# Performance work log

Hardware: AMD Instinct MI355X
Metric: run time of the kernel (lower is better)

## Reference

```python
import jax, jax.numpy as jnp
import numpy as np

B, K_SLOTS, P = 4096, 8, 768
SLOT = P // 3          # 256, slot feature dim
HID = 256              # pres/up hidden width
NC, NP = 512, 512
LN_EPS = 1e-5


def _layernorm(x, g, b):
    m = jnp.mean(x, axis=-1, keepdims=True)
    v = jnp.var(x, axis=-1, keepdims=True)
    return (x - m) * jax.lax.rsqrt(v + LN_EPS) * g + b


def _mlp2(x, W1, b1, g, bt, W2, b2):
    # Linear -> LayerNorm -> ReLU -> Linear (torchvision ops.MLP with hidden=[256, out])
    h = jax.nn.relu(_layernorm(x @ W1 + b1, g, bt))
    return h @ W2 + b2


def setup_inputs() -> dict:
    key = jax.random.key(0)
    ks = jax.random.split(key, 24)
    rn = lambda k, shp, s=1.0: jax.random.normal(k, shp, dtype=jnp.float32) * s
    d = {
        "inst_embed": rn(ks[0], (B, P)),
        "slots": rn(ks[1], (B, K_SLOTS, SLOT)),
        # fc / fp: single Linear(p, p)
        "Wfc": rn(ks[2], (P, P), 1.0 / np.sqrt(P)),
        "bfc": jnp.zeros((P,), jnp.float32),
        "Wfp": rn(ks[3], (P, P), 1.0 / np.sqrt(P)),
        "bfp": jnp.zeros((P,), jnp.float32),
        # memory codebooks (plain randn per the original)
        "Kc": rn(ks[4], (NC, P)),
        "Vc": rn(ks[5], (NC, P)),
        "Kp": rn(ks[6], (NP, P)),
        "Vp": rn(ks[7], (NP, P)),
        # pres MLP: Linear(4p/3,256)+LN+ReLU, Linear(256,p/3)
        "pres_W1": rn(ks[8], (SLOT + P, HID), 1.0 / np.sqrt(SLOT + P)),
        "pres_b1": jnp.zeros((HID,), jnp.float32),
        "pres_g": jnp.ones((HID,), jnp.float32),
        "pres_bt": jnp.zeros((HID,), jnp.float32),
        "pres_W2": rn(ks[9], (HID, SLOT), 1.0 / np.sqrt(HID)),
        "pres_b2": jnp.zeros((SLOT,), jnp.float32),
        # up MLP: same shapes
        "up_W1": rn(ks[10], (SLOT + P, HID), 1.0 / np.sqrt(SLOT + P)),
        "up_b1": jnp.zeros((HID,), jnp.float32),
        "up_g": jnp.ones((HID,), jnp.float32),
        "up_bt": jnp.zeros((HID,), jnp.float32),
        "up_W2": rn(ks[11], (HID, SLOT), 1.0 / np.sqrt(HID)),
        "up_b2": jnp.zeros((SLOT,), jnp.float32),
    }
    return d


def reference(inst_embed, slots, Wfc, bfc, Wfp, bfp, Kc, Vc, Kp, Vp,
              pres_W1, pres_b1, pres_g, pres_bt, pres_W2, pres_b2,
              up_W1, up_b1, up_g, up_bt, up_W2, up_b2):
    scale = jnp.float32(np.sqrt(P))
    # selection: soft attention over the two codebooks
    Qc = inst_embed @ Wfc + bfc                     # [B, P]
    Qp = inst_embed @ Wfp + bfp                     # [B, P]
    c = jax.nn.softmax(jnp.einsum('bi,ci->bc', Qc, Kc) / scale, axis=-1) @ Vc  # [B, P]
    p = jax.nn.softmax(jnp.einsum('bi,pi->bp', Qp, Kp) / scale, axis=-1) @ Vp  # [B, P]
    # update: vectorized over the K slot loop of the original
    cb = jnp.broadcast_to(c[:, None, :], (B, K_SLOTS, P))
    pb = jnp.broadcast_to(p[:, None, :], (B, K_SLOTS, P))
    hc = jnp.concatenate([slots, cb], axis=-1)      # [B, K, SLOT+P]
    hp = jnp.concatenate([slots, pb], axis=-1)      # [B, K, SLOT+P]
    gate_pres = _mlp2(hc, pres_W1, pres_b1, pres_g, pres_bt, pres_W2, pres_b2)
    gate_up = _mlp2(hp, up_W1, up_b1, up_g, up_bt, up_W2, up_b2)
    return slots + gate_pres * gate_up              # [B, K, SLOT]
```

## Files before the change

kernel.cpp:

```cpp
#include <hip/hip_runtime.h>
#include <stdint.h>

#define BB    4096
#define KS    8
#define PP    768
#define SLOT  256
#define HID   256
#define NC    512
#define BKROWS (BB*KS)
typedef unsigned short u16;
typedef short bf16x8 __attribute__((ext_vector_type(8)));
typedef float f32x4  __attribute__((ext_vector_type(4)));

__device__ __forceinline__ u16 f2bf(float x) {
  union { float f; uint32_t u; } v; v.f = x;
  return (u16)((v.u + 0x7FFFu + ((v.u >> 16) & 1u)) >> 16);
}

__device__ __forceinline__ u16 f2h(float x) {
  union { _Float16 h; u16 u; } cv; cv.h = (_Float16)x; return cv.u;
}
__device__ __forceinline__ float h2f(u16 x) {
  union { u16 u; _Float16 h; } cv; cv.u = x; return (float)cv.h;
}

__device__ __forceinline__ void gload_lds16(u16* ldst, const u16* gsrc) {
  __builtin_amdgcn_global_load_lds(
      (const __attribute__((address_space(1))) void*)gsrc,
      (__attribute__((address_space(3))) void*)ldst, 16, 0, 0);
}

template<int EPI>
__device__ __forceinline__ void gemm_core64(
    const u16* __restrict__ A, int lda,
    const u16* __restrict__ B, int ldb,
    const float* __restrict__ bias,
    void* __restrict__ out, int ldo, int K,
    int blockRow, int blockCol, u16* lsA, u16* lsB)
{
  const int tid  = threadIdx.x;
  const int w    = tid >> 6;
  const int lane = tid & 63;
  const int wm   = w >> 1, wn = w & 1;
  const int rl   = lane >> 4, cl = lane & 15;

  f32x4 acc[2][4];
  const f32x4 zero = {0.f, 0.f, 0.f, 0.f};
#pragma unroll
  for (int i = 0; i < 2; ++i)
#pragma unroll
    for (int j = 0; j < 4; ++j) acc[i][j] = zero;

  const u16* Ablk = A + (size_t)blockRow * lda;
  const u16* Bblk = B + (size_t)blockCol * ldb;

  for (int k0 = 0; k0 < K; k0 += 64) {
#pragma unroll
    for (int i = 0; i < 2; ++i) {
      int seg   = i * 4 + w;
      int off16 = seg * 64 + lane;
      int row   = off16 >> 3;
      int chunk = (off16 & 7) ^ (row & 7);
      gload_lds16(lsA + seg * 512, Ablk + (size_t)row * lda + k0 + chunk * 8);
    }
#pragma unroll
    for (int i = 0; i < 4; ++i) {
      int seg   = i * 4 + w;
      int off16 = seg * 64 + lane;
      int row   = off16 >> 3;
      int chunk = (off16 & 7) ^ (row & 7);
      gload_lds16(lsB + seg * 512, Bblk + (size_t)row * ldb + k0 + chunk * 8);
    }
    __syncthreads();

#pragma unroll
    for (int ks = 0; ks < 2; ++ks) {
      bf16x8 aF[2], bF[4];
#pragma unroll
      for (int f = 0; f < 2; ++f) {
        int r  = wm * 32 + f * 16 + cl;
        int ca = ((ks * 4 + rl) ^ (r & 7)) * 8;
        aF[f] = *(const bf16x8*)(lsA + r * 64 + ca);
      }
#pragma unroll
      for (int f = 0; f < 4; ++f) {
        int rn = wn * 64 + f * 16 + cl;
        int cb = ((ks * 4 + rl) ^ (rn & 7)) * 8;
        bF[f] = *(const bf16x8*)(lsB + rn * 64 + cb);
      }
#pragma unroll
      for (int fm = 0; fm < 2; ++fm)
#pragma unroll
        for (int fn = 0; fn < 4; ++fn)
          acc[fm][fn] = __builtin_amdgcn_mfma_f32_16x16x32_bf16(
              aF[fm], bF[fn], acc[fm][fn], 0, 0, 0);
    }
    __syncthreads();
  }

#pragma unroll
  for (int fm = 0; fm < 2; ++fm) {
#pragma unroll
    for (int fn = 0; fn < 4; ++fn) {
      f32x4 v = acc[fm][fn];
#pragma unroll
      for (int r = 0; r < 4; ++r) {
        int grow = blockRow + wm * 32 + fm * 16 + rl * 4 + r;
        int gcol = blockCol + wn * 64 + fn * 16 + cl;
        float x = v[r];
        if constexpr (EPI == 2) {
          ((u16*)out)[(size_t)grow * ldo + gcol] = f2bf(x);
        } else if constexpr (EPI == 3) {
          x += bias[gcol];
          ((float*)out)[(size_t)grow * ldo + gcol] = x;
        } else if constexpr (EPI == 5) {
          x += bias[gcol];
          ((u16*)out)[(size_t)grow * ldo + gcol] = f2h(x);
        }
      }
    }
  }
}

__device__ __forceinline__ void cvt_seg(const float* __restrict__ in,
                                        u16* __restrict__ outp, int b, int n4) {
  int i = b * 256 + threadIdx.x;
  if (i < n4) {
    float4 v = ((const float4*)in)[i];
    ushort4 o;
    o.x = f2bf(v.x); o.y = f2bf(v.y); o.z = f2bf(v.z); o.w = f2bf(v.w);
    ((ushort4*)outp)[i] = o;
  }
}

__device__ __forceinline__ void pack_seg(const float* __restrict__ s0,
                                         const float* __restrict__ s1,
                                         u16* __restrict__ dst, int b) {
  int br = b >> 4, ng = b & 15;
  const float* src = br ? s1 : s0;
  int w = threadIdx.x >> 6, lane = threadIdx.x & 63;
  int rl = lane >> 4, cl = lane & 15;
#pragma unroll
  for (int s = 0; s < 2; ++s) {
    int step = w * 2 + s;
    union { u16 u[8]; uint4 q; } o;
#pragma unroll
    for (int j = 0; j < 8; ++j)
      o.u[j] = f2bf(src[(size_t)(step * 32 + rl * 8 + j) * 256 + ng * 16 + cl]);
    *(uint4*)(dst + (size_t)(((br * 16 + ng) * 8 + step) * 64 + lane) * 8) = o.q;
  }
}

__global__ __launch_bounds__(256) void prep_all(
    const float* __restrict__ inst, const float* __restrict__ Kc,
    const float* __restrict__ Kp, const float* __restrict__ Wfc,
    const float* __restrict__ Wfp, const float* __restrict__ Vc,
    const float* __restrict__ Vp, const float* __restrict__ pW1,
    const float* __restrict__ uW1, const float* __restrict__ pW2,
    const float* __restrict__ uW2, const float* __restrict__ bfc,
    const float* __restrict__ bfp,
    u16* instb, u16* Kcb, u16* Kpb, u16* Wfcb, u16* Wfpb, u16* Vcb, u16* Vpb,
    u16* W1Tp, u16* W1Tu, u16* W1pk, u16* W2pk, float* sb)
{
  __shared__ float tile[32][33];
  int b = blockIdx.x;
  if (b < 3072)      { cvt_seg(inst, instb, b,        786432); return; }
  else if (b < 3456) { cvt_seg(Kc,   Kcb,   b - 3072,  98304); return; }
  else if (b < 3840) { cvt_seg(Kp,   Kpb,   b - 3456,  98304); return; }
  else if (b < 4416) { cvt_seg(Wfc,  Wfcb,  b - 3840, 147456); return; }
  else if (b < 4992) { cvt_seg(Wfp,  Wfpb,  b - 4416, 147456); return; }
  else if (b < 5376) { cvt_seg(Vc,   Vcb,   b - 4992,  98304); return; }
  else if (b < 5760) { cvt_seg(Vp,   Vpb,   b - 5376,  98304); return; }
  else if (b < 6272) {
    int bb = b - 5760;
    const float* in = (bb < 256) ? pW1 : uW1;
    u16* outp = (bb < 256) ? W1Tp : W1Tu;
    bb &= 255;
    int tc = (bb & 7) * 32, tr = (bb >> 3) * 32;
    int lx = threadIdx.x & 31, ly = threadIdx.x >> 5;
#pragma unroll
    for (int i = 0; i < 32; i += 8)
      tile[ly + i][lx] = in[(size_t)(tr + ly + i) * 256 + tc + lx];
    __syncthreads();
#pragma unroll
    for (int i = 0; i < 32; i += 8)
      outp[(size_t)(tc + ly + i) * 1024 + tr + lx] = f2bf(tile[lx][ly + i]);
    return;
  }
  else if (b < 6304) { pack_seg(pW1, uW1, W1pk, b - 6272); return; }
  else if (b < 6336) { pack_seg(pW2, uW2, W2pk, b - 6304); return; }
  else {
    int w = threadIdx.x >> 6, lane = threadIdx.x & 63;
    int row = (b - 6336) * 4 + w;
    int br = row >> 9, n = row & 511;
    const float* Kr = (br ? Kp : Kc) + (size_t)n * PP;
    const float* bf = br ? bfp : bfc;
    float s = 0.f;
#pragma unroll
    for (int j = 0; j < 12; ++j) s += Kr[lane + j * 64] * bf[lane + j * 64];
#pragma unroll
    for (int o = 32; o; o >>= 1) s += __shfl_xor(s, o);
    if (!lane) sb[row] = s;
  }
}

__global__ __launch_bounds__(256) void gemm_mixed(
    const u16* Kcb, const u16* Kpb, const u16* Wfcb, const u16* Wfpb,
    u16* KWc, u16* KWp,
    const u16* W1Tp, const u16* W1Tu, const u16* Vcb, const u16* Vpb,
    u16* VW1p, u16* VW1u)
{
  __shared__ u16 lsA[64 * 64];
  __shared__ u16 lsB[128 * 64];
  int b = blockIdx.x;
  if (b < 96) {
    int z = b / 48, r = b % 48;
    gemm_core64<2>(z ? Kpb : Kcb, PP, z ? Wfpb : Wfcb, PP, nullptr,
                   z ? KWp : KWc, PP, PP, (r & 7) * 64, (r >> 3) * 128, lsA, lsB);
  } else {
    int c = b - 96, z = c / 16, r = c % 16;
    gemm_core64<2>((z ? W1Tu : W1Tp) + 256, 1024, z ? Vpb : Vcb, PP, nullptr,
                   z ? VW1u : VW1p, NC, PP, (r & 3) * 64, (r >> 2) * 128, lsA, lsB);
  }
}

__global__ __launch_bounds__(256) void gemm_scores(
    const u16* instb, const u16* KW, const float* sb, u16* scH)
{
  __shared__ u16 lsA[64 * 64];
  __shared__ u16 lsB[128 * 64];
  gemm_core64<5>(instb, PP, KW, PP, sb, scH, 1024, PP,
                 blockIdx.x * 64, blockIdx.y * 128, lsA, lsB);
}

__global__ __launch_bounds__(256) void gemm_t(
    const u16* Pb, const u16* VW1p, const u16* VW1u,
    const float* pb1, const float* ub1, float* t0, float* t1)
{
  __shared__ u16 lsA[64 * 64];
  __shared__ u16 lsB[128 * 64];
  int z = blockIdx.z;
  gemm_core64<3>(Pb + (size_t)z * BB * NC, NC, z ? VW1u : VW1p, NC,
                 z ? ub1 : pb1, z ? t1 : t0, SLOT, NC,
                 blockIdx.x * 64, blockIdx.y * 128, lsA, lsB);
}

__global__ __launch_bounds__(256) void softmax_rows(const u16* __restrict__ scH,
                                                    u16* __restrict__ Pp) {
  int w = threadIdx.x >> 6, lane = threadIdx.x & 63;
  int row = blockIdx.x * 4 + w;
  int i = row >> 1, b = row & 1;
  const u16* src = scH + (size_t)i * 1024 + b * 512 + lane * 8;
  uint4 q = *(const uint4*)src;
  const u16* hp = (const u16*)&q;
  float vv[8];
#pragma unroll
  for (int j = 0; j < 8; ++j) vv[j] = h2f(hp[j]);
  float m = vv[0];
#pragma unroll
  for (int j = 1; j < 8; ++j) m = fmaxf(m, vv[j]);
#pragma unroll
  for (int o = 32; o; o >>= 1) m = fmaxf(m, __shfl_xor(m, o));
  const float alpha = 0.03608439182435161f;
  float e[8], s = 0.f;
#pragma unroll
  for (int j = 0; j < 8; ++j) { e[j] = __expf((vv[j] - m) * alpha); s += e[j]; }
#pragma unroll
  for (int o = 32; o; o >>= 1) s += __shfl_xor(s, o);
  float inv = 1.f / s;
  union { u16 u[8]; uint4 q; } ou;
#pragma unroll
  for (int j = 0; j < 8; ++j) ou.u[j] = f2bf(e[j] * inv);
  *(uint4*)(Pp + ((size_t)b * BB + i) * 512 + lane * 8) = ou.q;
}

__global__ __launch_bounds__(512, 4) void fused_update(
    const float* __restrict__ slots,
    const float* __restrict__ t0, const float* __restrict__ t1,
    const u16* __restrict__ W1pk, const u16* __restrict__ W2pk,
    const float* __restrict__ pg, const float* __restrict__ pbt,
    const float* __restrict__ ug, const float* __restrict__ ubt,
    const float* __restrict__ pb2, const float* __restrict__ ub2,
    float* __restrict__ outp)
{
  __shared__ u16 lsH[2][32 * 256];
  __shared__ float lstat[2][32][16];
  __shared__ float lfin[2][32][2];

  const int tid = threadIdx.x, w = tid >> 6, lane = tid & 63;
  const int rl = lane >> 4, cl = lane & 15;
  const int blockRow = blockIdx.x * 32;

  u16* lsA = lsH[0];

#pragma unroll
  for (int it = 0; it < 4; ++it) {
    int L = it * 512 + tid;
    int row = L >> 6, qc = L & 63;
    float4 v = *(const float4*)(slots + (size_t)(blockRow + row) * 256 + qc * 4);
    ushort4 b; b.x = f2bf(v.x); b.y = f2bf(v.y); b.z = f2bf(v.z); b.w = f2bf(v.w);
    int chunk = qc >> 1, half = qc & 1;
    *(ushort4*)(lsA + row * 256 + (((chunk ^ (row & 7)) << 3) + half * 4)) = b;
  }
  __syncthreads();

  f32x4 acc[2][4];
  const f32x4 zero = {0.f, 0.f, 0.f, 0.f};
#pragma unroll
  for (int i = 0; i < 2; ++i)
#pragma unroll
    for (int j = 0; j < 4; ++j) acc[i][j] = zero;

#define MF(A, B, C) C = __builtin_amdgcn_mfma_f32_16x16x32_bf16(A, B, C, 0, 0, 0);

  {
    bf16x8 pb[3][2], ub[3][2];
#define FR1(NG, S) (*(const bf16x8*)(W1pk + (size_t)(((NG) * 8 + (S)) * 64 + lane) * 8))
#define LDW1(SL, S) { pb[SL][0] = FR1(w * 2, S);      pb[SL][1] = FR1(w * 2 + 1, S);  \
                      ub[SL][0] = FR1(16 + w * 2, S); ub[SL][1] = FR1(17 + w * 2, S); \
                      asm volatile("" ::: "memory"); }
    LDW1(0, 0) LDW1(1, 1) LDW1(2, 2)
#pragma unroll
    for (int s = 0; s < 8; ++s) {
      const int sl = s % 3;
      bf16x8 a0 = *(const bf16x8*)(lsA + cl * 256 + (((s * 4 + rl) ^ (cl & 7)) << 3));
      bf16x8 a1 = *(const bf16x8*)(lsA + (16 + cl) * 256 + (((s * 4 + rl) ^ (cl & 7)) << 3));
      MF(a0, pb[sl][0], acc[0][0]) MF(a1, pb[sl][0], acc[1][0])
      MF(a0, pb[sl][1], acc[0][1]) MF(a1, pb[sl][1], acc[1][1])
      MF(a0, ub[sl][0], acc[0][2]) MF(a1, ub[sl][0], acc[1][2])
      MF(a0, ub[sl][1], acc[0][3]) MF(a1, ub[sl][1], acc[1][3])
      if (s < 5) LDW1(sl, s + 3)
    }
#undef LDW1
#undef FR1
  }

#pragma unroll
  for (int fm = 0; fm < 2; ++fm) {
    size_t trr = (size_t)(blockIdx.x * 4 + fm * 2 + (rl >> 1)) * 256;
#pragma unroll
    for (int fn = 0; fn < 2; ++fn) {
      int col = w * 32 + fn * 16 + cl;
      float tp = t0[trr + col], tu = t1[trr + col];
#pragma unroll
      for (int r = 0; r < 4; ++r) {
        acc[fm][fn][r]     += tp;
        acc[fm][2 + fn][r] += tu;
      }
    }
  }

#pragma unroll
  for (int fm = 0; fm < 2; ++fm)
#pragma unroll
    for (int br = 0; br < 2; ++br) {
      f32x4 s = acc[fm][br * 2] + acc[fm][br * 2 + 1];
      f32x4 q = acc[fm][br * 2] * acc[fm][br * 2] + acc[fm][br * 2 + 1] * acc[fm][br * 2 + 1];
#pragma unroll
      for (int o = 1; o < 16; o <<= 1) {
#pragma unroll
        for (int r = 0; r < 4; ++r) {
          s[r] += __shfl_xor(s[r], o);
          q[r] += __shfl_xor(q[r], o);
        }
      }
      if (cl == 0) {
#pragma unroll
        for (int r = 0; r < 4; ++r) {
          int row = fm * 16 + rl * 4 + r;
          lstat[br][row][w]     = s[r];
          lstat[br][row][8 + w] = q[r];
        }
      }
    }
  __syncthreads();

  if (tid < 64) {
    int fb = tid >> 5, row = tid & 31;
    f32x4 a = *(const f32x4*)&lstat[fb][row][0];
    f32x4 b = *(const f32x4*)&lstat[fb][row][4];
    f32x4 c = *(const f32x4*)&lstat[fb][row][8];
    f32x4 d = *(const f32x4*)&lstat[fb][row][12];
    float ss = a[0] + a[1] + a[2] + a[3] + b[0] + b[1] + b[2] + b[3];
    float qq = c[0] + c[1] + c[2] + c[3] + d[0] + d[1] + d[2] + d[3];
    float mu = ss * (1.f / 256.f);
    lfin[fb][row][0] = mu;
    lfin[fb][row][1] = rsqrtf(qq * (1.f / 256.f) - mu * mu + 1e-5f);
  }
  __syncthreads();

  {
    float gv[2][2], btv[2][2];
#pragma unroll
    for (int fn = 0; fn < 2; ++fn) {
      int col = w * 32 + fn * 16 + cl;
      gv[0][fn] = pg[col];  btv[0][fn] = pbt[col];
      gv[1][fn] = ug[col];  btv[1][fn] = ubt[col];
    }
#pragma unroll
    for (int fm = 0; fm < 2; ++fm) {
      float mean[2][4], rstd[2][4];
#pragma unroll
      for (int r = 0; r < 4; ++r) {
        int row = fm * 16 + rl * 4 + r;
        mean[0][r] = lfin[0][row][0]; rstd[0][r] = lfin[0][row][1];
        mean[1][r] = lfin[1][row][0]; rstd[1][r] = lfin[1][row][1];
      }
#pragma unroll
      for (int br = 0; br < 2; ++br)
#pragma unroll
        for (int fn = 0; fn < 2; ++fn) {
          int col = w * 32 + fn * 16 + cl;
#pragma unroll
          for (int r = 0; r < 4; ++r) {
            int row = fm * 16 + rl * 4 + r;
            float h = fmaxf((acc[fm][br * 2 + fn][r] - mean[br][r]) * rstd[br][r]
                            * gv[br][fn] + btv[br][fn], 0.f);
            lsH[br][row * 256 + (((col >> 3) ^ (row & 7)) << 3) + (col & 7)] = f2bf(h);
          }
        }
    }
  }
#pragma unroll
  for (int i = 0; i < 2; ++i)
#pragma unroll
    for (int j = 0; j < 4; ++j) acc[i][j] = zero;
  __syncthreads();

  const int brw = w >> 2, wc = w & 3;
  const u16* hsrc = lsH[brw];
  const float* b2src = brw ? ub2 : pb2;
  float b2v[4];
#pragma unroll
  for (int fn = 0; fn < 4; ++fn) b2v[fn] = b2src[wc * 64 + fn * 16 + cl];

  {
    bf16x8 bq[3][4];
#define FR2(NG, S) (*(const bf16x8*)(W2pk + (size_t)(((NG) * 8 + (S)) * 64 + lane) * 8))
#define LDW2(SL, S) { bq[SL][0] = FR2(brw * 16 + wc * 4,     S); \
                      bq[SL][1] = FR2(brw * 16 + wc * 4 + 1, S); \
                      bq[SL][2] = FR2(brw * 16 + wc * 4 + 2, S); \
                      bq[SL][3] = FR2(brw * 16 + wc * 4 + 3, S); \
                      asm volatile("" ::: "memory"); }
    LDW2(0, 0) LDW2(1, 1) LDW2(2, 2)
#pragma unroll
    for (int s = 0; s < 8; ++s) {
      const int sl = s % 3;
      bf16x8 a0 = *(const bf16x8*)(hsrc + cl * 256 + (((s * 4 + rl) ^ (cl & 7)) << 3));
      bf16x8 a1 = *(const bf16x8*)(hsrc + (16 + cl) * 256 + (((s * 4 + rl) ^ (cl & 7)) << 3));
      MF(a0, bq[sl][0], acc[0][0]) MF(a1, bq[sl][0], acc[1][0])
      MF(a0, bq[sl][1], acc[0][1]) MF(a1, bq[sl][1], acc[1][1])
      MF(a0, bq[sl][2], acc[0][2]) MF(a1, bq[sl][2], acc[1][2])
      MF(a0, bq[sl][3], acc[0][3]) MF(a1, bq[sl][3], acc[1][3])
      if (s < 5) LDW2(sl, s + 3)
    }
#undef LDW2
#undef FR2
  }
#undef MF
  __syncthreads();

  float* xbuf = (float*)&lsH[0][0];
  const int base = wc * 2048;
  if (brw == 0) {
#pragma unroll
    for (int fm = 0; fm < 2; ++fm)
#pragma unroll
      for (int fn = 0; fn < 4; ++fn)
#pragma unroll
        for (int r = 0; r < 4; ++r)
          xbuf[base + ((fm * 4 + fn) * 4 + r) * 64 + lane] = acc[fm][fn][r] + b2v[fn];
  }
  __syncthreads();

  if (brw == 1) {
#pragma unroll
    for (int fm = 0; fm < 2; ++fm)
#pragma unroll
      for (int fn = 0; fn < 4; ++fn)
#pragma unroll
        for (int r = 0; r < 4; ++r) {
          float gp = xbuf[base + ((fm * 4 + fn) * 4 + r) * 64 + lane];
          float gu = acc[fm][fn][r] + b2v[fn];
          int row = blockRow + fm * 16 + rl * 4 + r;
          int col = wc * 64 + fn * 16 + cl;
          size_t idx = (size_t)row * 256 + col;
          outp[idx] = slots[idx] + gp * gu;
        }
  }
}

extern "C" void kernel_launch(void* const* d_in, const int* in_sizes, int n_in,
                              void* d_out, int out_size, void* d_ws, size_t ws_size,
                              hipStream_t stream) {
  const float* inst  = (const float*)d_in[0];
  const float* slots = (const float*)d_in[1];
  const float* Wfc   = (const float*)d_in[2];
  const float* bfc   = (const float*)d_in[3];
  const float* Wfp   = (const float*)d_in[4];
  const float* bfp   = (const float*)d_in[5];
  const float* Kc    = (const float*)d_in[6];
  const float* Vc    = (const float*)d_in[7];
  const float* Kp    = (const float*)d_in[8];
  const float* Vp    = (const float*)d_in[9];
  const float* pW1   = (const float*)d_in[10];
  const float* pb1   = (const float*)d_in[11];
  const float* pg    = (const float*)d_in[12];
  const float* pbt   = (const float*)d_in[13];
  const float* pW2   = (const float*)d_in[14];
  const float* pb2   = (const float*)d_in[15];
  const float* uW1   = (const float*)d_in[16];
  const float* ub1   = (const float*)d_in[17];
  const float* ug    = (const float*)d_in[18];
  const float* ubt   = (const float*)d_in[19];
  const float* uW2   = (const float*)d_in[20];
  const float* ub2   = (const float*)d_in[21];
  float* out = (float*)d_out;
  char*  ws  = (char*)d_ws;

  const size_t OFF_INST  = 0;
  const size_t OFF_KC    = OFF_INST  + 6291456;
  const size_t OFF_KP    = OFF_KC    + 786432;
  const size_t OFF_WFCB  = OFF_KP    + 786432;
  const size_t OFF_WFPB  = OFF_WFCB  + 1179648;
  const size_t OFF_VCB   = OFF_WFPB  + 1179648;
  const size_t OFF_VPB   = OFF_VCB   + 786432;
  const size_t OFF_W1TP  = OFF_VPB   + 786432;
  const size_t OFF_W1TU  = OFF_W1TP  + 524288;
  const size_t OFF_W1PK  = OFF_W1TU  + 524288;
  const size_t OFF_W2PK  = OFF_W1PK  + 262144;
  const size_t OFF_KW    = OFF_W2PK  + 262144;
  const size_t OFF_VW1   = OFF_KW    + 1572864;
  const size_t OFF_SB    = OFF_VW1   + 524288;
  const size_t OFF_T     = OFF_SB    + 4096;
  const size_t OFF_SC    = OFF_T     + 8388608;
  const size_t OFF_P     = OFF_SC    + 8388608;

  u16*   instb = (u16*)(ws + OFF_INST);
  u16*   Kcb   = (u16*)(ws + OFF_KC);
  u16*   Kpb   = (u16*)(ws + OFF_KP);
  u16*   Wfcb  = (u16*)(ws + OFF_WFCB);
  u16*   Wfpb  = (u16*)(ws + OFF_WFPB);
  u16*   Vcb   = (u16*)(ws + OFF_VCB);
  u16*   Vpb   = (u16*)(ws + OFF_VPB);
  u16*   W1Tp  = (u16*)(ws + OFF_W1TP);
  u16*   W1Tu  = (u16*)(ws + OFF_W1TU);
  u16*   W1pk  = (u16*)(ws + OFF_W1PK);
  u16*   W2pk  = (u16*)(ws + OFF_W2PK);
  u16*   KWc   = (u16*)(ws + OFF_KW);
  u16*   KWp   = KWc + (size_t)NC * PP;
  u16*   VW1p  = (u16*)(ws + OFF_VW1);
  u16*   VW1u  = VW1p + (size_t)SLOT * NC;
  float* sb    = (float*)(ws + OFF_SB);
  float* t0    = (float*)(ws + OFF_T);
  float* t1    = t0 + (size_t)BB * SLOT;
  u16*   scH   = (u16*)(ws + OFF_SC);
  u16*   Pb    = (u16*)(ws + OFF_P);

  prep_all<<<dim3(6592), 256, 0, stream>>>(
      inst, Kc, Kp, Wfc, Wfp, Vc, Vp, pW1, uW1, pW2, uW2, bfc, bfp,
      instb, Kcb, Kpb, Wfcb, Wfpb, Vcb, Vpb, W1Tp, W1Tu, W1pk, W2pk, sb);

  gemm_mixed<<<dim3(128), 256, 0, stream>>>(
      Kcb, Kpb, Wfcb, Wfpb, KWc, KWp, W1Tp, W1Tu, Vcb, Vpb, VW1p, VW1u);

  gemm_scores<<<dim3(64, 8), 256, 0, stream>>>(instb, KWc, sb, scH);

  softmax_rows<<<dim3(2048), 256, 0, stream>>>(scH, Pb);

  gemm_t<<<dim3(64, 2, 2), 256, 0, stream>>>(Pb, VW1p, VW1u, pb1, ub1, t0, t1);

  fused_update<<<dim3(1024), 512, 0, stream>>>(
      slots, t0, t1, W1pk, W2pk, pg, pbt, ug, ubt, pb2, ub2, out);

  (void)in_sizes; (void)n_in; (void)out_size; (void)ws_size;
}
```

Baseline: 89.56 us.

## Align second-GEMM column split so each wave computes both gates, drop LDS exchange

The second MLP layer now gives each wave matching pres and up output columns, so gate_pres*gate_up is formed in registers instead of going through an LDS buffer with two extra barriers. The residual slots values, the t0/t1 first-layer terms, and the LN/bias parameters are prefetched before the first GEMM so their global latency overlaps the MFMA work. In exchange each wave reads A fragments from both hidden buffers, doubling LDS reads in the second GEMM, and holds more live registers across the GEMMs, which could reduce occupancy.

```diff
diff --git a/kernel.cpp b/kernel.cpp
--- a/kernel.cpp
+++ b/kernel.cpp
@@ -302,6 +302,32 @@
     int chunk = qc >> 1, half = qc & 1;
     *(ushort4*)(lsA + row * 256 + (((chunk ^ (row & 7)) << 3) + half * 4)) = b;
   }
+
+  float tp_[2][2], tu_[2][2];
+  float gv[2][2], btv[2][2];
+  float b2p[2], b2u[2];
+  float spre[2][2][4];
+#pragma unroll
+  for (int fm = 0; fm < 2; ++fm) {
+    size_t trr = (size_t)(blockIdx.x * 4 + fm * 2 + (rl >> 1)) * 256;
+#pragma unroll
+    for (int fn = 0; fn < 2; ++fn) {
+      int col = w * 32 + fn * 16 + cl;
+      tp_[fm][fn] = t0[trr + col];
+      tu_[fm][fn] = t1[trr + col];
+#pragma unroll
+      for (int r = 0; r < 4; ++r)
+        spre[fm][fn][r] = slots[(size_t)(blockRow + fm * 16 + rl * 4 + r) * 256 + col];
+    }
+  }
+#pragma unroll
+  for (int fn = 0; fn < 2; ++fn) {
+    int col = w * 32 + fn * 16 + cl;
+    gv[0][fn] = pg[col];  btv[0][fn] = pbt[col];
+    gv[1][fn] = ug[col];  btv[1][fn] = ubt[col];
+    b2p[fn] = pb2[col];   b2u[fn] = ub2[col];
+  }
+  asm volatile("" ::: "memory");
   __syncthreads();
 
   f32x4 acc[2][4];
@@ -336,19 +362,14 @@
   }
 
 #pragma unroll
-  for (int fm = 0; fm < 2; ++fm) {
-    size_t trr = (size_t)(blockIdx.x * 4 + fm * 2 + (rl >> 1)) * 256;
-#pragma unroll
-    for (int fn = 0; fn < 2; ++fn) {
-      int col = w * 32 + fn * 16 + cl;
-      float tp = t0[trr + col], tu = t1[trr + col];
+  for (int fm = 0; fm < 2; ++fm)
+#pragma unroll
+    for (int fn = 0; fn < 2; ++fn)
 #pragma unroll
       for (int r = 0; r < 4; ++r) {
-        acc[fm][fn][r]     += tp;
-        acc[fm][2 + fn][r] += tu;
-      }
-    }
-  }
+        acc[fm][fn][r]     += tp_[fm][fn];
+        acc[fm][2 + fn][r] += tu_[fm][fn];
+      }
 
 #pragma unroll
   for (int fm = 0; fm < 2; ++fm)
@@ -390,13 +411,6 @@
   __syncthreads();
 
   {
-    float gv[2][2], btv[2][2];
-#pragma unroll
-    for (int fn = 0; fn < 2; ++fn) {
-      int col = w * 32 + fn * 16 + cl;
-      gv[0][fn] = pg[col];  btv[0][fn] = pbt[col];
-      gv[1][fn] = ug[col];  btv[1][fn] = ubt[col];
-    }
 #pragma unroll
     for (int fm = 0; fm < 2; ++fm) {
       float mean[2][4], rstd[2][4];
@@ -427,67 +441,43 @@
     for (int j = 0; j < 4; ++j) acc[i][j] = zero;
   __syncthreads();
 
-  const int brw = w >> 2, wc = w & 3;
-  const u16* hsrc = lsH[brw];
-  const float* b2src = brw ? ub2 : pb2;
-  float b2v[4];
-#pragma unroll
-  for (int fn = 0; fn < 4; ++fn) b2v[fn] = b2src[wc * 64 + fn * 16 + cl];
-
   {
-    bf16x8 bq[3][4];
+    bf16x8 qp[3][2], qu[3][2];
 #define FR2(NG, S) (*(const bf16x8*)(W2pk + (size_t)(((NG) * 8 + (S)) * 64 + lane) * 8))
-#define LDW2(SL, S) { bq[SL][0] = FR2(brw * 16 + wc * 4,     S); \
-                      bq[SL][1] = FR2(brw * 16 + wc * 4 + 1, S); \
-                      bq[SL][2] = FR2(brw * 16 + wc * 4 + 2, S); \
-                      bq[SL][3] = FR2(brw * 16 + wc * 4 + 3, S); \
+#define LDW2(SL, S) { qp[SL][0] = FR2(w * 2, S);      qp[SL][1] = FR2(w * 2 + 1, S);  \
+                      qu[SL][0] = FR2(16 + w * 2, S); qu[SL][1] = FR2(17 + w * 2, S); \
                       asm volatile("" ::: "memory"); }
     LDW2(0, 0) LDW2(1, 1) LDW2(2, 2)
 #pragma unroll
     for (int s = 0; s < 8; ++s) {
       const int sl = s % 3;
-      bf16x8 a0 = *(const bf16x8*)(hsrc + cl * 256 + (((s * 4 + rl) ^ (cl & 7)) << 3));
-      bf16x8 a1 = *(const bf16x8*)(hsrc + (16 + cl) * 256 + (((s * 4 + rl) ^ (cl & 7)) << 3));
-      MF(a0, bq[sl][0], acc[0][0]) MF(a1, bq[sl][0], acc[1][0])
-      MF(a0, bq[sl][1], acc[0][1]) MF(a1, bq[sl][1], acc[1][1])
-      MF(a0, bq[sl][2], acc[0][2]) MF(a1, bq[sl][2], acc[1][2])
-      MF(a0, bq[sl][3], acc[0][3]) MF(a1, bq[sl][3], acc[1][3])
+      bf16x8 aP0 = *(const bf16x8*)(lsH[0] + cl * 256 + (((s * 4 + rl) ^ (cl & 7)) << 3));
+      bf16x8 aP1 = *(const bf16x8*)(lsH[0] + (16 + cl) * 256 + (((s * 4 + rl) ^ (cl & 7)) << 3));
+      bf16x8 aU0 = *(const bf16x8*)(lsH[1] + cl * 256 + (((s * 4 + rl) ^ (cl & 7)) << 3));
+      bf16x8 aU1 = *(const bf16x8*)(lsH[1] + (16 + cl) * 256 + (((s * 4 + rl) ^ (cl & 7)) << 3));
+      MF(aP0, qp[sl][0], acc[0][0]) MF(aP1, qp[sl][0], acc[1][0])
+      MF(aP0, qp[sl][1], acc[0][1]) MF(aP1, qp[sl][1], acc[1][1])
+      MF(aU0, qu[sl][0], acc[0][2]) MF(aU1, qu[sl][0], acc[1][2])
+      MF(aU0, qu[sl][1], acc[0][3]) MF(aU1, qu[sl][1], acc[1][3])
       if (s < 5) LDW2(sl, s + 3)
     }
 #undef LDW2
 #undef FR2
   }
 #undef MF
-  __syncthreads();
-
-  float* xbuf = (float*)&lsH[0][0];
-  const int base = wc * 2048;
-  if (brw == 0) {
-#pragma unroll
-    for (int fm = 0; fm < 2; ++fm)
-#pragma unroll
-      for (int fn = 0; fn < 4; ++fn)
-#pragma unroll
-        for (int r = 0; r < 4; ++r)
-          xbuf[base + ((fm * 4 + fn) * 4 + r) * 64 + lane] = acc[fm][fn][r] + b2v[fn];
-  }
-  __syncthreads();
-
-  if (brw == 1) {
-#pragma unroll
-    for (int fm = 0; fm < 2; ++fm)
-#pragma unroll
-      for (int fn = 0; fn < 4; ++fn)
-#pragma unroll
-        for (int r = 0; r < 4; ++r) {
-          float gp = xbuf[base + ((fm * 4 + fn) * 4 + r) * 64 + lane];
-          float gu = acc[fm][fn][r] + b2v[fn];
-          int row = blockRow + fm * 16 + rl * 4 + r;
-          int col = wc * 64 + fn * 16 + cl;
-          size_t idx = (size_t)row * 256 + col;
-          outp[idx] = slots[idx] + gp * gu;
-        }
-  }
+
+#pragma unroll
+  for (int fm = 0; fm < 2; ++fm)
+#pragma unroll
+    for (int fn = 0; fn < 2; ++fn)
+#pragma unroll
+      for (int r = 0; r < 4; ++r) {
+        float gp = acc[fm][fn][r]     + b2p[fn];
+        float gu = acc[fm][2 + fn][r] + b2u[fn];
+        int row = blockRow + fm * 16 + rl * 4 + r;
+        int col = w * 32 + fn * 16 + cl;
+        outp[(size_t)row * 256 + col] = spre[fm][fn][r] + gp * gu;
+      }
 }
 
 extern "C" void kernel_launch(void* const* d_in, const int* in_sizes, int n_in,
```

New measurement: 125.6 us. 40.2% more time.
